# Kernel optimization log

Hardware: AMD Instinct MI355X
Metric: run time of the kernel (lower is better)

Reference implementation:

```python
import jax, jax.numpy as jnp
import numpy as np

N = 4096        # num_nodes == num_messages (required by the einsum contraction)
HID = 256       # hidden_dim
MD = 32         # message_dim (per-head dim)
H = 8           # num_heads


def setup_inputs() -> dict:
    key = jax.random.key(0)
    ks = jax.random.split(key, 12)
    s = 0.02
    return {
        "node_features": jax.random.normal(ks[0], (N, HID), dtype=jnp.float32),
        "messages": jax.random.normal(ks[1], (N, MD), dtype=jnp.float32),
        "adjacency": jax.random.randint(ks[2], (N, N), 0, 2, dtype=jnp.int32),
        "Wq": jax.random.normal(ks[3], (HID, H * MD), dtype=jnp.float32) * s,
        "bq": jnp.zeros((H * MD,), dtype=jnp.float32),
        "Wk": jax.random.normal(ks[4], (HID, H * MD), dtype=jnp.float32) * s,
        "bk": jnp.zeros((H * MD,), dtype=jnp.float32),
        "Wv": jax.random.normal(ks[5], (MD, H * MD), dtype=jnp.float32) * s,
        "bv": jnp.zeros((H * MD,), dtype=jnp.float32),
        "Wo": jax.random.normal(ks[6], (H * MD, MD), dtype=jnp.float32) * s,
        "bo": jnp.zeros((MD,), dtype=jnp.float32),
    }


def reference(node_features, messages, adjacency, Wq, bq, Wk, bk, Wv, bv, Wo, bo):
    n = node_features.shape[0]
    m = messages.shape[0]
    # projections; view(num, H, -1) splits the H*MD output as [H, MD]
    Q = (node_features @ Wq + bq).reshape(n, H, MD)   # [n, h, d]
    K = (node_features @ Wk + bk).reshape(n, H, MD)   # [m, h, d] (m == n)
    V = (messages @ Wv + bv).reshape(m, H, MD)        # [m, h, d]
    scale = 1.0 / np.sqrt(MD).astype(np.float32)
    scores = jnp.einsum('nhd,mhd->nmh', Q, K) * scale  # [n, m, h]
    # adjacency mask: masked_fill(mask == 0, -1e9)
    scores = jnp.where((adjacency == 0)[:, :, None], jnp.float32(-1e9), scores)
    attn = jax.nn.softmax(scores, axis=1)              # softmax over m
    routed = jnp.einsum('nmh,mhd->nhd', attn, V).reshape(n, H * MD)
    routed = routed @ Wo + bo                          # [n, MD]
    return routed, attn.mean(axis=-1)                  # ([n, MD], [n, m])
```

## Files before the change

### kernel.cpp

```cpp
#include <hip/hip_runtime.h>
#include <math.h>

#define NN 4096
#define HID 256
#define MD 32
#define NH 8
#define SCALE 0.17677669529663687f

typedef float f32x4 __attribute__((ext_vector_type(4)));
typedef short bf16x8 __attribute__((ext_vector_type(8)));
typedef _Float16 f16x4 __attribute__((ext_vector_type(4)));
typedef _Float16 f16x2 __attribute__((ext_vector_type(2)));

__device__ inline unsigned int bfr(float x) {
    unsigned int u = __float_as_uint(x);
    return (u + 0x7fffu + ((u >> 16) & 1u)) >> 16;
}
__device__ inline unsigned int pkbf(float a, float b) {
    return bfr(a) | (bfr(b) << 16);
}
__device__ inline unsigned int pkhf(float a, float b) {
    union { f16x2 h; unsigned int u; } z;
    z.h = (f16x2){(_Float16)a, (_Float16)b};
    return z.u;
}

__global__ __launch_bounds__(256, 2) void proj_qk(
    const float* __restrict__ nf,
    const float* __restrict__ Wq, const float* __restrict__ bq,
    const float* __restrict__ Wk, const float* __restrict__ bk,
    unsigned short* __restrict__ Qb, unsigned short* __restrict__ Kb)
{
    __shared__ __align__(16) float inT[256 * 20];
    __shared__ __align__(16) float Wc[16 * 256];
    const int b = blockIdx.x;
    const int isK = b >> 8;
    const int nb = b & 255;
    const float* W = isK ? Wk : Wq;
    const float* bias = isK ? bk : bq;
    unsigned short* outp = isK ? Kb : Qb;
    const int t = threadIdx.x;
    const int rg = t >> 6;
    const int j4 = t & 63;

    for (int i = t; i < 1024; i += 256) {
        int row = i >> 6, kq = i & 63;
        float4 v = *(const float4*)(nf + (size_t)(nb * 16 + row) * 256 + kq * 4);
        inT[(kq * 4 + 0) * 20 + row] = v.x;
        inT[(kq * 4 + 1) * 20 + row] = v.y;
        inT[(kq * 4 + 2) * 20 + row] = v.z;
        inT[(kq * 4 + 3) * 20 + row] = v.w;
    }
    float acc[4][4];
    #pragma unroll
    for (int r = 0; r < 4; ++r)
        #pragma unroll
        for (int d = 0; d < 4; ++d) acc[r][d] = 0.f;

    for (int kc = 0; kc < 16; ++kc) {
        __syncthreads();
        for (int i = t; i < 1024; i += 256)
            *(float4*)&Wc[i * 4] = *(const float4*)(W + (size_t)kc * 4096 + i * 4);
        __syncthreads();
        #pragma unroll 4
        for (int k = 0; k < 16; ++k) {
            float4 iv = *(const float4*)&inT[(kc * 16 + k) * 20 + rg * 4];
            float4 wv = *(const float4*)&Wc[k * 256 + j4 * 4];
            acc[0][0] += iv.x * wv.x; acc[0][1] += iv.x * wv.y;
            acc[0][2] += iv.x * wv.z; acc[0][3] += iv.x * wv.w;
            acc[1][0] += iv.y * wv.x; acc[1][1] += iv.y * wv.y;
            acc[1][2] += iv.y * wv.z; acc[1][3] += iv.y * wv.w;
            acc[2][0] += iv.z * wv.x; acc[2][1] += iv.z * wv.y;
            acc[2][2] += iv.z * wv.z; acc[2][3] += iv.z * wv.w;
            acc[3][0] += iv.w * wv.x; acc[3][1] += iv.w * wv.y;
            acc[3][2] += iv.w * wv.z; acc[3][3] += iv.w * wv.w;
        }
    }
    const float sc = isK ? 1.0f : SCALE;
    const float4 bv = *(const float4*)(bias + j4 * 4);
    const int c0 = j4 * 4, h = c0 >> 5, d = c0 & 31;
    #pragma unroll
    for (int r = 0; r < 4; ++r) {
        int n = nb * 16 + rg * 4 + r;
        float v0 = (acc[r][0] + bv.x) * sc;
        float v1 = (acc[r][1] + bv.y) * sc;
        float v2 = (acc[r][2] + bv.z) * sc;
        float v3 = (acc[r][3] + bv.w) * sc;
        uint2 o;
        o.x = pkbf(v0, v1); o.y = pkbf(v2, v3);
        *(uint2*)(outp + ((size_t)h * NN + n) * 32 + d) = o;
    }
}

__global__ __launch_bounds__(256) void proj_v(
    const float* __restrict__ msg, const float* __restrict__ Wv,
    const float* __restrict__ bv, float* __restrict__ Vo)
{
    __shared__ __align__(16) float in_lds[32 * 32];
    const int nb = blockIdx.x;
    const int t = threadIdx.x;
    {
        int i = t;
        ((float4*)in_lds)[i] = ((const float4*)(msg + (size_t)nb * 1024))[i];
    }
    __syncthreads();
    float acc[32];
    #pragma unroll
    for (int r = 0; r < 32; ++r) acc[r] = 0.f;
    #pragma unroll 8
    for (int k = 0; k < 32; ++k) {
        float w = Wv[k * 256 + t];
        #pragma unroll
        for (int r = 0; r < 32; ++r) acc[r] += in_lds[r * 32 + k] * w;
    }
    const float bb = bv[t];
    #pragma unroll
    for (int r = 0; r < 32; ++r)
        Vo[(size_t)(nb * 32 + r) * 256 + t] = acc[r] + bb;
}

__global__ __launch_bounds__(256) void abit_kernel(
    const int* __restrict__ adj, unsigned long long* __restrict__ abit)
{
    const int n = blockIdx.x * 4 + (threadIdx.x >> 6);
    const int l = threadIdx.x & 63;
    for (int j = 0; j < 64; ++j) {
        int v = adj[(size_t)n * NN + j * 64 + l];
        unsigned long long m = __ballot(v != 0);
        if (l == 0) abit[(size_t)n * 64 + j] = m;
    }
}

__global__ __launch_bounds__(256) void pack_vt(
    const float* __restrict__ Vf, unsigned short* __restrict__ Vt, int usef16)
{
    __shared__ __align__(16) float lds[128 * 33];
    const int h = blockIdx.x >> 5, mt = blockIdx.x & 31;
    const int t = threadIdx.x;
    for (int k = 0; k < 4; ++k) {
        int flat = k * 256 + t;
        int row = flat >> 3, c4 = flat & 7;
        float4 v = *(const float4*)(Vf + (size_t)(mt * 128 + row) * 256 + h * 32 + c4 * 4);
        lds[row * 33 + c4 * 4 + 0] = v.x;
        lds[row * 33 + c4 * 4 + 1] = v.y;
        lds[row * 33 + c4 * 4 + 2] = v.z;
        lds[row * 33 + c4 * 4 + 3] = v.w;
    }
    __syncthreads();
    const int d = t >> 3, mq = t & 7;
    #pragma unroll
    for (int k = 0; k < 2; ++k) {
        int m0 = mq * 16 + k * 8;
        uint4 o;
        if (usef16) {
            o.x = pkhf(lds[(m0 + 0) * 33 + d], lds[(m0 + 1) * 33 + d]);
            o.y = pkhf(lds[(m0 + 2) * 33 + d], lds[(m0 + 3) * 33 + d]);
            o.z = pkhf(lds[(m0 + 4) * 33 + d], lds[(m0 + 5) * 33 + d]);
            o.w = pkhf(lds[(m0 + 6) * 33 + d], lds[(m0 + 7) * 33 + d]);
        } else {
            o.x = pkbf(lds[(m0 + 0) * 33 + d], lds[(m0 + 1) * 33 + d]);
            o.y = pkbf(lds[(m0 + 2) * 33 + d], lds[(m0 + 3) * 33 + d]);
            o.z = pkbf(lds[(m0 + 4) * 33 + d], lds[(m0 + 5) * 33 + d]);
            o.w = pkbf(lds[(m0 + 6) * 33 + d], lds[(m0 + 7) * 33 + d]);
        }
        *(uint4*)(Vt + ((size_t)(h * 32 + d)) * NN + mt * 128 + m0) = o;
    }
}

__global__ __launch_bounds__(256, 4) void sweep1s_kernel(
    const unsigned short* __restrict__ Qb, const unsigned short* __restrict__ Kb,
    const unsigned int* __restrict__ abit, float* __restrict__ Lpart)
{
    __shared__ __align__(16) char smem[32768];
    const int nquad = blockIdx.x, msg = blockIdx.y;
    const int t = threadIdx.x;
    const int w = t >> 6, l = t & 63;
    const int g = l >> 4, q = l & 15;
    const int n0 = nquad * 64 + w * 16;
    const int m0 = msg * 512;
    const int fq = (q >> 1) & 3;

    const char* gsrc[4];
    #pragma unroll
    for (int i = 0; i < 4; ++i) {
        int s = i * 256 + t;
        int tile = s >> 7;
        int r = (s >> 2) & 31;
        int gr = (s & 3) ^ ((r >> 1) & 3);
        gsrc[i] = (const char*)Kb + (((size_t)tile * NN + m0 + r) * 64 + gr * 16);
    }
    const unsigned int* abrow = abit + (size_t)(n0 + q) * 128 + msg * 16;

    bf16x8 qf[8];
    #pragma unroll
    for (int h = 0; h < 8; ++h)
        qf[h] = *(const bf16x8*)(Qb + (((size_t)h * NN + n0 + q) << 5) + g * 8);
    float lacc[8];
    #pragma unroll
    for (int h = 0; h < 8; ++h) lacc[h] = 0.f;

    #pragma unroll
    for (int i = 0; i < 4; ++i)
        __builtin_amdgcn_global_load_lds((const unsigned int*)gsrc[i],
            (unsigned int*)(smem + i * 4096 + w * 1024), 16, 0, 0);
    unsigned int wb = abrow[0];
    unsigned int wbn = 0;
    __syncthreads();

    for (int c = 0; c < 16; ++c) {
        const char* cur = smem + (c & 1) * 16384;
        if (c < 15) {
            wbn = abrow[c + 1];
            char* nxt = smem + ((c & 1) ^ 1) * 16384;
            #pragma unroll
            for (int i = 0; i < 4; ++i)
                __builtin_amdgcn_global_load_lds(
                    (const unsigned int*)(gsrc[i] + (size_t)(c + 1) * 2048),
                    (unsigned int*)(nxt + i * 4096 + w * 1024), 16, 0, 0);
        }
        #pragma unroll
        for (int h = 0; h < 8; ++h) {
            const int ko = h * 2048 + q * 64 + ((g ^ fq) << 4);
            bf16x8 ka0 = *(const bf16x8*)(cur + ko);
            bf16x8 ka1 = *(const bf16x8*)(cur + ko + 1024);
            f32x4 z = {0.f, 0.f, 0.f, 0.f};
            f32x4 s0 = __builtin_amdgcn_mfma_f32_16x16x32_bf16(ka0, qf[h], z, 0, 0, 0);
            f32x4 s1 = __builtin_amdgcn_mfma_f32_16x16x32_bf16(ka1, qf[h], z, 0, 0, 0);
            #pragma unroll
            for (int r = 0; r < 4; ++r) {
                float e0 = __expf(s0[r]);
                float e1 = __expf(s1[r]);
                lacc[h] += ((wb >> (4 * g + r)) & 1u) ? e0 : 0.f;
                lacc[h] += ((wb >> (16 + 4 * g + r)) & 1u) ? e1 : 0.f;
            }
        }
        __syncthreads();
        wb = wbn;
    }
    #pragma unroll
    for (int h = 0; h < 8; ++h) {
        float v = lacc[h];
        v += __shfl_xor(v, 16);
        v += __shfl_xor(v, 32);
        if (g == 0) Lpart[(size_t)msg * 32768 + h * NN + n0 + q] = v;
    }
}

__global__ __launch_bounds__(256, 2) void sweep2s_kernel(
    const unsigned short* __restrict__ Qb, const unsigned short* __restrict__ Kb,
    const unsigned short* __restrict__ Vt, const unsigned int* __restrict__ abit,
    const float* __restrict__ Linv, float* __restrict__ Opart,
    float* __restrict__ amean)
{
    __shared__ __align__(16) char smem[65536];
    const int nquad = blockIdx.x, msg = blockIdx.y;
    const int t = threadIdx.x;
    const int w = t >> 6, l = t & 63;
    const int g = l >> 4, q = l & 15;
    const int n0 = nquad * 64 + w * 16;
    const int m0 = msg * 512;
    const int fq = (q >> 1) & 3;

    const char* gsrc[8];
    unsigned int gstep[8];
    #pragma unroll
    for (int i = 0; i < 8; ++i) {
        int s = i * 256 + t;
        int tile = s >> 7;
        int r = (s >> 2) & 31;
        int gr = (s & 3) ^ ((r >> 1) & 3);
        if (tile < 8) {
            gsrc[i] = (const char*)Kb + (((size_t)tile * NN + m0 + r) * 64 + gr * 16);
            gstep[i] = 2048;
        } else {
            gsrc[i] = (const char*)Vt + ((((size_t)(tile - 8) * 32 + r) * NN + m0) * 2 + gr * 16);
            gstep[i] = 64;
        }
    }
    const unsigned int* abrow = abit + (size_t)(n0 + q) * 128 + msg * 16;

    bf16x8 qf[8];
    float rL[8];
    #pragma unroll
    for (int h = 0; h < 8; ++h) {
        qf[h] = *(const bf16x8*)(Qb + (((size_t)h * NN + n0 + q) << 5) + g * 8);
        rL[h] = Linv[h * NN + n0 + q];
    }
    f32x4 o[8][2];
    #pragma unroll
    for (int h = 0; h < 8; ++h) {
        o[h][0] = (f32x4){0.f, 0.f, 0.f, 0.f};
        o[h][1] = (f32x4){0.f, 0.f, 0.f, 0.f};
    }

    #pragma unroll
    for (int i = 0; i < 8; ++i)
        __builtin_amdgcn_global_load_lds((const unsigned int*)gsrc[i],
            (unsigned int*)(smem + i * 4096 + w * 1024), 16, 0, 0);
    unsigned int wb = abrow[0];
    unsigned int wbn = 0;
    __syncthreads();

    for (int c = 0; c < 16; ++c) {
        const char* cur = smem + (c & 1) * 32768;
        if (c < 15) {
            wbn = abrow[c + 1];
            char* nxt = smem + ((c & 1) ^ 1) * 32768;
            #pragma unroll
            for (int i = 0; i < 8; ++i)
                __builtin_amdgcn_global_load_lds(
                    (const unsigned int*)(gsrc[i] + (size_t)(c + 1) * gstep[i]),
                    (unsigned int*)(nxt + i * 4096 + w * 1024), 16, 0, 0);
        }
        const int mb = m0 + c * 32;
        float am[8];
        #pragma unroll
        for (int r = 0; r < 8; ++r) am[r] = 0.f;

        #pragma unroll
        for (int h = 0; h < 8; ++h) {
            const int ko = h * 2048 + q * 64 + ((g ^ fq) << 4);
            bf16x8 ka0 = *(const bf16x8*)(cur + ko);
            bf16x8 ka1 = *(const bf16x8*)(cur + ko + 1024);
            const int vbase = (8 + h) * 2048 + q * 64 + (g & 1) * 8;
            const int vo0 = vbase + (((g >> 1) ^ fq) << 4);
            const int vo1 = vbase + (((2 + (g >> 1)) ^ fq) << 4);
            f16x4 va00 = *(const f16x4*)(cur + vo0);
            f16x4 va01 = *(const f16x4*)(cur + vo0 + 1024);
            f16x4 va10 = *(const f16x4*)(cur + vo1);
            f16x4 va11 = *(const f16x4*)(cur + vo1 + 1024);
            f32x4 z = {0.f, 0.f, 0.f, 0.f};
            f32x4 s0 = __builtin_amdgcn_mfma_f32_16x16x32_bf16(ka0, qf[h], z, 0, 0, 0);
            f32x4 s1 = __builtin_amdgcn_mfma_f32_16x16x32_bf16(ka1, qf[h], z, 0, 0, 0);
            float pn[8];
            #pragma unroll
            for (int r = 0; r < 4; ++r) {
                float e0 = __expf(s0[r]) * rL[h];
                float e1 = __expf(s1[r]) * rL[h];
                pn[r]     = ((wb >> (4 * g + r)) & 1u) ? e0 : 0.f;
                pn[4 + r] = ((wb >> (16 + 4 * g + r)) & 1u) ? e1 : 0.f;
                am[r] += pn[r];
                am[4 + r] += pn[4 + r];
            }
            union { unsigned int u[2]; f16x4 v; } pA, pB;
            pA.u[0] = pkhf(pn[0], pn[1]); pA.u[1] = pkhf(pn[2], pn[3]);
            pB.u[0] = pkhf(pn[4], pn[5]); pB.u[1] = pkhf(pn[6], pn[7]);
            o[h][0] = __builtin_amdgcn_mfma_f32_16x16x16f16(va00, pA.v, o[h][0], 0, 0, 0);
            o[h][1] = __builtin_amdgcn_mfma_f32_16x16x16f16(va01, pA.v, o[h][1], 0, 0, 0);
            o[h][0] = __builtin_amdgcn_mfma_f32_16x16x16f16(va10, pB.v, o[h][0], 0, 0, 0);
            o[h][1] = __builtin_amdgcn_mfma_f32_16x16x16f16(va11, pB.v, o[h][1], 0, 0, 0);
        }
        float4 a0, a1;
        a0.x = am[0] * 0.125f; a0.y = am[1] * 0.125f;
        a0.z = am[2] * 0.125f; a0.w = am[3] * 0.125f;
        a1.x = am[4] * 0.125f; a1.y = am[5] * 0.125f;
        a1.z = am[6] * 0.125f; a1.w = am[7] * 0.125f;
        *(float4*)(amean + (size_t)(n0 + q) * NN + mb + 4 * g) = a0;
        *(float4*)(amean + (size_t)(n0 + q) * NN + mb + 16 + 4 * g) = a1;
        __syncthreads();
        wb = wbn;
    }

    float* op = Opart + ((size_t)msg * NN + n0 + q) * 256;
    #pragma unroll
    for (int h = 0; h < 8; ++h) {
        *(f32x4*)(op + h * 32 + 4 * g) = o[h][0];
        *(f32x4*)(op + h * 32 + 16 + 4 * g) = o[h][1];
    }
}

__global__ __launch_bounds__(256, 4) void sweep1_old(
    const unsigned short* __restrict__ Qb, const unsigned short* __restrict__ Kb,
    const unsigned int* __restrict__ abit, float* __restrict__ Lpart)
{
    const int ntile = blockIdx.x, msg = blockIdx.y;
    const int t = threadIdx.x;
    const int w = t >> 6, l = t & 63;
    const int g = l >> 4, q = l & 15;
    const int ms = msg * 4 + w;
    const int n0 = ntile * 16;
    const int mbase = ms * 256;
    bf16x8 qf[8];
    #pragma unroll
    for (int h = 0; h < 8; ++h)
        qf[h] = *(const bf16x8*)(Qb + (((size_t)h * NN + n0 + q) << 5) + g * 8);
    float lacc[8];
    #pragma unroll
    for (int h = 0; h < 8; ++h) lacc[h] = 0.f;
    for (int ch = 0; ch < 8; ++ch) {
        const int mb = mbase + ch * 32;
        const unsigned int wbits = abit[(size_t)(n0 + q) * 128 + (mb >> 5)];
        #pragma unroll
        for (int h = 0; h < 8; ++h) {
            bf16x8 ka0 = *(const bf16x8*)(Kb + (((size_t)h * NN + mb + q) << 5) + g * 8);
            bf16x8 ka1 = *(const bf16x8*)(Kb + (((size_t)h * NN + mb + 16 + q) << 5) + g * 8);
            f32x4 z = {0.f, 0.f, 0.f, 0.f};
            f32x4 s0 = __builtin_amdgcn_mfma_f32_16x16x32_bf16(ka0, qf[h], z, 0, 0, 0);
            f32x4 s1 = __builtin_amdgcn_mfma_f32_16x16x32_bf16(ka1, qf[h], z, 0, 0, 0);
            #pragma unroll
            for (int r = 0; r < 4; ++r) {
                float e0 = __expf(s0[r]);
                float e1 = __expf(s1[r]);
                lacc[h] += ((wbits >> (4 * g + r)) & 1u) ? e0 : 0.f;
                lacc[h] += ((wbits >> (16 + 4 * g + r)) & 1u) ? e1 : 0.f;
            }
        }
    }
    #pragma unroll
    for (int h = 0; h < 8; ++h) {
        float v = lacc[h];
        v += __shfl_xor(v, 16);
        v += __shfl_xor(v, 32);
        if (g == 0) Lpart[(size_t)ms * 32768 + h * NN + n0 + q] = v;
    }
}

__global__ __launch_bounds__(256, 2) void sweep2_old(
    const unsigned short* __restrict__ Qb, const unsigned short* __restrict__ Kb,
    const unsigned short* __restrict__ Vt, const unsigned int* __restrict__ abit,
    const float* __restrict__ Linv, float* __restrict__ Opart,
    float* __restrict__ amean)
{
    __shared__ __align__(16) float Ow[2 * 16 * 260];
    const int ntile = blockIdx.x, msg = blockIdx.y;
    const int t = threadIdx.x;
    const int w = t >> 6, l = t & 63;
    const int g = l >> 4, q = l & 15;
    const int ms = msg * 4 + w;
    const int n0 = ntile * 16;
    const int mbase = ms * 256;
    const int baddr = (q + (g & 1) * 32) << 2;
    const bool hi = (g >= 2);
    bf16x8 qf[8];
    float rL[8];
    #pragma unroll
    for (int h = 0; h < 8; ++h) {
        qf[h] = *(const bf16x8*)(Qb + (((size_t)h * NN + n0 + q) << 5) + g * 8);
        rL[h] = Linv[h * NN + n0 + q];
    }
    f32x4 o[8][2];
    #pragma unroll
    for (int h = 0; h < 8; ++h) {
        o[h][0] = (f32x4){0.f, 0.f, 0.f, 0.f};
        o[h][1] = (f32x4){0.f, 0.f, 0.f, 0.f};
    }
    for (int ch = 0; ch < 8; ++ch) {
        const int mb = mbase + ch * 32;
        const unsigned int wbits = abit[(size_t)(n0 + q) * 128 + (mb >> 5)];
        float am[8];
        #pragma unroll
        for (int r = 0; r < 8; ++r) am[r] = 0.f;
        #pragma unroll
        for (int h = 0; h < 8; ++h) {
            bf16x8 ka0 = *(const bf16x8*)(Kb + (((size_t)h * NN + mb + q) << 5) + g * 8);
            bf16x8 ka1 = *(const bf16x8*)(Kb + (((size_t)h * NN + mb + 16 + q) << 5) + g * 8);
            f32x4 z = {0.f, 0.f, 0.f, 0.f};
            f32x4 s0 = __builtin_amdgcn_mfma_f32_16x16x32_bf16(ka0, qf[h], z, 0, 0, 0);
            f32x4 s1 = __builtin_amdgcn_mfma_f32_16x16x32_bf16(ka1, qf[h], z, 0, 0, 0);
            float pn[8];
            #pragma unroll
            for (int r = 0; r < 4; ++r) {
                float e0 = __expf(s0[r]) * rL[h];
                float e1 = __expf(s1[r]) * rL[h];
                pn[r]     = ((wbits >> (4 * g + r)) & 1u) ? e0 : 0.f;
                pn[4 + r] = ((wbits >> (16 + 4 * g + r)) & 1u) ? e1 : 0.f;
                am[r] += pn[r];
                am[4 + r] += pn[4 + r];
            }
            unsigned int pk0 = pkbf(pn[0], pn[1]);
            unsigned int pk1 = pkbf(pn[2], pn[3]);
            unsigned int pk2 = pkbf(pn[4], pn[5]);
            unsigned int pk3 = pkbf(pn[6], pn[7]);
            int r0lo = __builtin_amdgcn_ds_bpermute(baddr,      (int)pk0);
            int r0hi = __builtin_amdgcn_ds_bpermute(baddr,      (int)pk2);
            int r1lo = __builtin_amdgcn_ds_bpermute(baddr,      (int)pk1);
            int r1hi = __builtin_amdgcn_ds_bpermute(baddr,      (int)pk3);
            int r2lo = __builtin_amdgcn_ds_bpermute(baddr + 64, (int)pk0);
            int r2hi = __builtin_amdgcn_ds_bpermute(baddr + 64, (int)pk2);
            int r3lo = __builtin_amdgcn_ds_bpermute(baddr + 64, (int)pk1);
            int r3hi = __builtin_amdgcn_ds_bpermute(baddr + 64, (int)pk3);
            union { unsigned int u[4]; bf16x8 v; } pu;
            pu.u[0] = (unsigned int)(hi ? r0hi : r0lo);
            pu.u[1] = (unsigned int)(hi ? r1hi : r1lo);
            pu.u[2] = (unsigned int)(hi ? r2hi : r2lo);
            pu.u[3] = (unsigned int)(hi ? r3hi : r3lo);
            bf16x8 va0 = *(const bf16x8*)(Vt + ((size_t)(h * 32 + q)) * NN + mb + g * 8);
            bf16x8 va1 = *(const bf16x8*)(Vt + ((size_t)(h * 32 + 16 + q)) * NN + mb + g * 8);
            o[h][0] = __builtin_amdgcn_mfma_f32_16x16x32_bf16(va0, pu.v, o[h][0], 0, 0, 0);
            o[h][1] = __builtin_amdgcn_mfma_f32_16x16x32_bf16(va1, pu.v, o[h][1], 0, 0, 0);
        }
        float4 a0, a1;
        a0.x = am[0] * 0.125f; a0.y = am[1] * 0.125f;
        a0.z = am[2] * 0.125f; a0.w = am[3] * 0.125f;
        a1.x = am[4] * 0.125f; a1.y = am[5] * 0.125f;
        a1.z = am[6] * 0.125f; a1.w = am[7] * 0.125f;
        *(float4*)(amean + (size_t)(n0 + q) * NN + mb + 4 * g) = a0;
        *(float4*)(amean + (size_t)(n0 + q) * NN + mb + 16 + 4 * g) = a1;
    }
    if (w < 2) {
        #pragma unroll
        for (int h = 0; h < 8; ++h)
            #pragma unroll
            for (int dt = 0; dt < 2; ++dt)
                *(f32x4*)&Ow[w * 4160 + q * 260 + h * 32 + dt * 16 + 4 * g] = o[h][dt];
    }
    __syncthreads();
    if (w >= 2) {
        #pragma unroll
        for (int h = 0; h < 8; ++h)
            #pragma unroll
            for (int dt = 0; dt < 2; ++dt) {
                f32x4* p = (f32x4*)&Ow[(w - 2) * 4160 + q * 260 + h * 32 + dt * 16 + 4 * g];
                *p = *p + o[h][dt];
            }
    }
    __syncthreads();
    for (int i = t; i < 4096; i += 256) {
        int n = i >> 8, c2 = i & 255;
        float v = Ow[n * 260 + c2] + Ow[4160 + n * 260 + c2];
        Opart[((size_t)msg * NN + n0 + n) * 256 + c2] = v;
    }
}

__global__ __launch_bounds__(256) void linv_kernel(
    const float* __restrict__ Lpart, float* __restrict__ Linv, int nms)
{
    int i = blockIdx.x * 256 + threadIdx.x;
    float s = 0.f;
    for (int ms = 0; ms < nms; ++ms) s += Lpart[(size_t)ms * 32768 + i];
    Linv[i] = 1.0f / s;
}

__global__ __launch_bounds__(256) void final_kernel(
    const float* __restrict__ Opart, const float* __restrict__ Wo,
    const float* __restrict__ bo, float* __restrict__ routed, int nms)
{
    __shared__ __align__(16) float Osum[16 * 260];
    __shared__ __align__(16) float WoT[32 * 260];
    const int nb = blockIdx.x, t = threadIdx.x;
    for (int i4 = t; i4 < 2048; i4 += 256) {
        int k = i4 >> 3, j4b = i4 & 7;
        float4 v = *(const float4*)(Wo + k * 32 + j4b * 4);
        WoT[(j4b * 4 + 0) * 260 + k] = v.x;
        WoT[(j4b * 4 + 1) * 260 + k] = v.y;
        WoT[(j4b * 4 + 2) * 260 + k] = v.z;
        WoT[(j4b * 4 + 3) * 260 + k] = v.w;
    }
    for (int i = t; i < 4096; i += 256) {
        int r = i >> 8, c = i & 255;
        const float* ap = Opart + ((size_t)(nb * 16 + r)) * 256 + c;
        float s = 0.f;
        for (int ms = 0; ms < nms; ++ms) s += ap[(size_t)ms * 1048576];
        Osum[r * 260 + c] = s;
    }
    __syncthreads();
    const int rh = t >> 5, j = t & 31;
    const float bj = bo[j];
    #pragma unroll
    for (int rr = 0; rr < 2; ++rr) {
        int r = rh * 2 + rr;
        float a0 = 0.f, a1 = 0.f;
        #pragma unroll
        for (int i4 = 0; i4 < 64; i4 += 2) {
            float4 ov = *(const float4*)&Osum[r * 260 + i4 * 4];
            float4 wv = *(const float4*)&WoT[j * 260 + i4 * 4];
            a0 += ov.x * wv.x + ov.y * wv.y + ov.z * wv.z + ov.w * wv.w;
            float4 ov2 = *(const float4*)&Osum[r * 260 + i4 * 4 + 4];
            float4 wv2 = *(const float4*)&WoT[j * 260 + i4 * 4 + 4];
            a1 += ov2.x * wv2.x + ov2.y * wv2.y + ov2.z * wv2.z + ov2.w * wv2.w;
        }
        routed[(size_t)(nb * 16 + r) * 32 + j] = a0 + a1 + bj;
    }
}

extern "C" void kernel_launch(void* const* d_in, const int* in_sizes, int n_in,
                              void* d_out, int out_size, void* d_ws, size_t ws_size,
                              hipStream_t stream) {
    const float* nf  = (const float*)d_in[0];
    const float* msg = (const float*)d_in[1];
    const int*   adj = (const int*)d_in[2];
    const float* Wq  = (const float*)d_in[3];
    const float* bq  = (const float*)d_in[4];
    const float* Wk  = (const float*)d_in[5];
    const float* bk  = (const float*)d_in[6];
    const float* Wv  = (const float*)d_in[7];
    const float* bv  = (const float*)d_in[8];
    const float* Wo  = (const float*)d_in[9];
    const float* bo  = (const float*)d_in[10];

    float* routed = (float*)d_out;
    float* amean  = (float*)d_out + (size_t)NN * MD;
    float* ws = (float*)d_ws;

    const bool bigws = (ws_size >= 43122688ull);

    if (bigws) {
        float* Vf = ws;
        float* Opart = ws;
        unsigned short* Qb = (unsigned short*)(ws + 8388608);
        unsigned short* Kb = (unsigned short*)(ws + 8912896);
        unsigned short* Vt = (unsigned short*)(ws + 9437184);
        unsigned int*   ab32 = (unsigned int*)(ws + 9961472);
        unsigned long long* ab64 = (unsigned long long*)(ws + 9961472);
        float* Lpart = ws + 10485760;
        float* Linv  = ws + 10747904;

        proj_qk<<<512, 256, 0, stream>>>(nf, Wq, bq, Wk, bk, Qb, Kb);
        proj_v<<<128, 256, 0, stream>>>(msg, Wv, bv, Vf);
        abit_kernel<<<1024, 256, 0, stream>>>(adj, ab64);
        pack_vt<<<256, 256, 0, stream>>>(Vf, Vt, 1);
        sweep1s_kernel<<<dim3(64, 8), 256, 0, stream>>>(Qb, Kb, ab32, Lpart);
        linv_kernel<<<128, 256, 0, stream>>>(Lpart, Linv, 8);
        sweep2s_kernel<<<dim3(64, 8), 256, 0, stream>>>(Qb, Kb, Vt, ab32, Linv, Opart, amean);
        final_kernel<<<256, 256, 0, stream>>>(Opart, Wo, bo, routed, 8);
    } else {
        float* Vf = ws;
        float* Opart = ws;
        unsigned short* Qb = (unsigned short*)(ws + 4194304);
        unsigned short* Kb = (unsigned short*)(ws + 4718592);
        unsigned short* Vt = (unsigned short*)(ws + 5242880);
        unsigned int*   ab32 = (unsigned int*)(ws + 5767168);
        unsigned long long* ab64 = (unsigned long long*)(ws + 5767168);
        float* Lpart = ws + 6291456;
        float* Linv  = ws + 6815744;

        proj_qk<<<512, 256, 0, stream>>>(nf, Wq, bq, Wk, bk, Qb, Kb);
        proj_v<<<128, 256, 0, stream>>>(msg, Wv, bv, Vf);
        abit_kernel<<<1024, 256, 0, stream>>>(adj, ab64);
        pack_vt<<<256, 256, 0, stream>>>(Vf, Vt, 0);
        sweep1_old<<<dim3(256, 4), 256, 0, stream>>>(Qb, Kb, ab32, Lpart);
        linv_kernel<<<128, 256, 0, stream>>>(Lpart, Linv, 16);
        sweep2_old<<<dim3(256, 4), 256, 0, stream>>>(Qb, Kb, Vt, ab32, Linv, Opart, amean);
        final_kernel<<<128, 256, 0, stream>>>(Opart, Wo, bo, routed, 4);
    }
}
```

Before: 197.5 us.

## Move Q/K projection to bf16 MFMA, vectorize mask packing, widen V fragment loads

Replaces the scalar-FMA Q/K projection with a bf16 conversion/transposition prep kernel followed by an MFMA-based projection. It also rewrites the adjacency bitmask kernel to read int4 per lane and interleave the bits, and updates the sweep kernels' mask bit indexing to match. The V transpose now uses an interleaved layout so sweep2 can fetch V with single 16-byte loads instead of four 8-byte ones. This adds an extra launch, and node features and weights are rounded to bf16 before the projection rather than only after, which slightly reduces precision.

```diff
diff --git a/kernel.cpp b/kernel.cpp
--- a/kernel.cpp
+++ b/kernel.cpp
@@ -9,6 +9,7 @@
 
 typedef float f32x4 __attribute__((ext_vector_type(4)));
 typedef short bf16x8 __attribute__((ext_vector_type(8)));
+typedef _Float16 f16x8 __attribute__((ext_vector_type(8)));
 typedef _Float16 f16x4 __attribute__((ext_vector_type(4)));
 typedef _Float16 f16x2 __attribute__((ext_vector_type(2)));
 
@@ -25,69 +26,93 @@
     return z.u;
 }
 
-__global__ __launch_bounds__(256, 2) void proj_qk(
-    const float* __restrict__ nf,
-    const float* __restrict__ Wq, const float* __restrict__ bq,
-    const float* __restrict__ Wk, const float* __restrict__ bk,
+__global__ __launch_bounds__(256) void prep_kernel(
+    const float* __restrict__ nf, const float* __restrict__ Wq,
+    const float* __restrict__ Wk, unsigned short* __restrict__ NFb,
+    unsigned short* __restrict__ Wt)
+{
+    __shared__ __align__(16) float lds[64 * 65];
+    const int b = blockIdx.x, t = threadIdx.x;
+    if (b < 512) {
+        const float* src = nf + (size_t)b * 2048 + t * 8;
+        float4 a = ((const float4*)src)[0];
+        float4 c = ((const float4*)src)[1];
+        uint4 o;
+        o.x = pkbf(a.x, a.y); o.y = pkbf(a.z, a.w);
+        o.z = pkbf(c.x, c.y); o.w = pkbf(c.z, c.w);
+        *(uint4*)(NFb + (size_t)b * 2048 + t * 8) = o;
+        return;
+    }
+    const int b2 = b - 512;
+    const int mat = b2 >> 4, tile = b2 & 15;
+    const int k0 = (tile >> 2) * 64, c0 = (tile & 3) * 64;
+    const float* W = mat ? Wk : Wq;
+    #pragma unroll
+    for (int i = 0; i < 16; ++i) {
+        int idx = i * 256 + t;
+        int row = idx >> 4, c4 = idx & 15;
+        float4 v = *(const float4*)(W + (size_t)(k0 + row) * 256 + c0 + c4 * 4);
+        lds[row * 65 + c4 * 4 + 0] = v.x;
+        lds[row * 65 + c4 * 4 + 1] = v.y;
+        lds[row * 65 + c4 * 4 + 2] = v.z;
+        lds[row * 65 + c4 * 4 + 3] = v.w;
+    }
+    __syncthreads();
+    #pragma unroll
+    for (int i = 0; i < 2; ++i) {
+        int j = i * 256 + t;
+        int c_loc = j >> 3, kq = j & 7;
+        uint4 o;
+        o.x = pkbf(lds[(kq * 8 + 0) * 65 + c_loc], lds[(kq * 8 + 1) * 65 + c_loc]);
+        o.y = pkbf(lds[(kq * 8 + 2) * 65 + c_loc], lds[(kq * 8 + 3) * 65 + c_loc]);
+        o.z = pkbf(lds[(kq * 8 + 4) * 65 + c_loc], lds[(kq * 8 + 5) * 65 + c_loc]);
+        o.w = pkbf(lds[(kq * 8 + 6) * 65 + c_loc], lds[(kq * 8 + 7) * 65 + c_loc]);
+        *(uint4*)(Wt + (size_t)mat * 65536 + (size_t)(c0 + c_loc) * 256 + k0 + kq * 8) = o;
+    }
+}
+
+__global__ __launch_bounds__(256, 4) void proj_mfma(
+    const unsigned short* __restrict__ NFb, const unsigned short* __restrict__ Wt,
+    const float* __restrict__ bq, const float* __restrict__ bk,
     unsigned short* __restrict__ Qb, unsigned short* __restrict__ Kb)
 {
-    __shared__ __align__(16) float inT[256 * 20];
-    __shared__ __align__(16) float Wc[16 * 256];
     const int b = blockIdx.x;
-    const int isK = b >> 8;
-    const int nb = b & 255;
-    const float* W = isK ? Wk : Wq;
+    const int isK = b >> 7, nb = b & 127;
+    const unsigned short* Wm = Wt + (size_t)isK * 65536;
     const float* bias = isK ? bk : bq;
     unsigned short* outp = isK ? Kb : Qb;
-    const int t = threadIdx.x;
-    const int rg = t >> 6;
-    const int j4 = t & 63;
-
-    for (int i = t; i < 1024; i += 256) {
-        int row = i >> 6, kq = i & 63;
-        float4 v = *(const float4*)(nf + (size_t)(nb * 16 + row) * 256 + kq * 4);
-        inT[(kq * 4 + 0) * 20 + row] = v.x;
-        inT[(kq * 4 + 1) * 20 + row] = v.y;
-        inT[(kq * 4 + 2) * 20 + row] = v.z;
-        inT[(kq * 4 + 3) * 20 + row] = v.w;
-    }
-    float acc[4][4];
-    #pragma unroll
-    for (int r = 0; r < 4; ++r)
-        #pragma unroll
-        for (int d = 0; d < 4; ++d) acc[r][d] = 0.f;
-
-    for (int kc = 0; kc < 16; ++kc) {
-        __syncthreads();
-        for (int i = t; i < 1024; i += 256)
-            *(float4*)&Wc[i * 4] = *(const float4*)(W + (size_t)kc * 4096 + i * 4);
-        __syncthreads();
-        #pragma unroll 4
-        for (int k = 0; k < 16; ++k) {
-            float4 iv = *(const float4*)&inT[(kc * 16 + k) * 20 + rg * 4];
-            float4 wv = *(const float4*)&Wc[k * 256 + j4 * 4];
-            acc[0][0] += iv.x * wv.x; acc[0][1] += iv.x * wv.y;
-            acc[0][2] += iv.x * wv.z; acc[0][3] += iv.x * wv.w;
-            acc[1][0] += iv.y * wv.x; acc[1][1] += iv.y * wv.y;
-            acc[1][2] += iv.y * wv.z; acc[1][3] += iv.y * wv.w;
-            acc[2][0] += iv.z * wv.x; acc[2][1] += iv.z * wv.y;
-            acc[2][2] += iv.z * wv.z; acc[2][3] += iv.z * wv.w;
-            acc[3][0] += iv.w * wv.x; acc[3][1] += iv.w * wv.y;
-            acc[3][2] += iv.w * wv.z; acc[3][3] += iv.w * wv.w;
+    const int t = threadIdx.x, w = t >> 6, l = t & 63;
+    const int g = l >> 4, q = l & 15;
+    const int n0 = nb * 32 + (w & 1) * 16;
+    const int chalf = w >> 1;
+
+    f32x4 acc[8];
+    #pragma unroll
+    for (int ct = 0; ct < 8; ++ct) acc[ct] = (f32x4){0.f, 0.f, 0.f, 0.f};
+
+    #pragma unroll
+    for (int kc = 0; kc < 8; ++kc) {
+        bf16x8 bfrag = *(const bf16x8*)(NFb + (size_t)(n0 + q) * 256 + kc * 32 + g * 8);
+        #pragma unroll
+        for (int ct = 0; ct < 8; ++ct) {
+            int c = (chalf * 8 + ct) * 16 + q;
+            bf16x8 afrag = *(const bf16x8*)(Wm + (size_t)c * 256 + kc * 32 + g * 8);
+            acc[ct] = __builtin_amdgcn_mfma_f32_16x16x32_bf16(afrag, bfrag, acc[ct], 0, 0, 0);
         }
     }
     const float sc = isK ? 1.0f : SCALE;
-    const float4 bv = *(const float4*)(bias + j4 * 4);
-    const int c0 = j4 * 4, h = c0 >> 5, d = c0 & 31;
-    #pragma unroll
-    for (int r = 0; r < 4; ++r) {
-        int n = nb * 16 + rg * 4 + r;
-        float v0 = (acc[r][0] + bv.x) * sc;
-        float v1 = (acc[r][1] + bv.y) * sc;
-        float v2 = (acc[r][2] + bv.z) * sc;
-        float v3 = (acc[r][3] + bv.w) * sc;
+    const int n = n0 + q;
+    #pragma unroll
+    for (int ct = 0; ct < 8; ++ct) {
+        int c0 = (chalf * 8 + ct) * 16 + 4 * g;
+        float4 bv = *(const float4*)(bias + c0);
+        float v0 = (acc[ct][0] + bv.x) * sc;
+        float v1 = (acc[ct][1] + bv.y) * sc;
+        float v2 = (acc[ct][2] + bv.z) * sc;
+        float v3 = (acc[ct][3] + bv.w) * sc;
         uint2 o;
         o.x = pkbf(v0, v1); o.y = pkbf(v2, v3);
+        int h = c0 >> 5, d = c0 & 31;
         *(uint2*)(outp + ((size_t)h * NN + n) * 32 + d) = o;
     }
 }
@@ -99,10 +124,7 @@
     __shared__ __align__(16) float in_lds[32 * 32];
     const int nb = blockIdx.x;
     const int t = threadIdx.x;
-    {
-        int i = t;
-        ((float4*)in_lds)[i] = ((const float4*)(msg + (size_t)nb * 1024))[i];
-    }
+    ((float4*)in_lds)[t] = ((const float4*)(msg + (size_t)nb * 1024))[t];
     __syncthreads();
     float acc[32];
     #pragma unroll
@@ -120,14 +142,25 @@
 }
 
 __global__ __launch_bounds__(256) void abit_kernel(
-    const int* __restrict__ adj, unsigned long long* __restrict__ abit)
-{
-    const int n = blockIdx.x * 4 + (threadIdx.x >> 6);
-    const int l = threadIdx.x & 63;
-    for (int j = 0; j < 64; ++j) {
-        int v = adj[(size_t)n * NN + j * 64 + l];
-        unsigned long long m = __ballot(v != 0);
-        if (l == 0) abit[(size_t)n * 64 + j] = m;
+    const int* __restrict__ adj, unsigned int* __restrict__ ab32)
+{
+    const int w = threadIdx.x >> 6, lane = threadIdx.x & 63;
+    const int n = blockIdx.x * 4 + w;
+    const int* base = adj + (size_t)n * NN;
+    for (int it = 0; it < 16; ++it) {
+        int4 v = *(const int4*)(base + it * 256 + lane * 4);
+        unsigned long long b0 = __ballot(v.x != 0);
+        unsigned long long b1 = __ballot(v.y != 0);
+        unsigned long long b2 = __ballot(v.z != 0);
+        unsigned long long b3 = __ballot(v.w != 0);
+        if (lane < 8) {
+            unsigned int sh = lane * 8;
+            unsigned int wd = (unsigned int)((b0 >> sh) & 0xffULL)
+                            | ((unsigned int)((b1 >> sh) & 0xffULL) << 8)
+                            | ((unsigned int)((b2 >> sh) & 0xffULL) << 16)
+                            | ((unsigned int)((b3 >> sh) & 0xffULL) << 24);
+            ab32[(size_t)n * 128 + it * 8 + lane] = wd;
+        }
     }
 }
 
@@ -147,23 +180,32 @@
         lds[row * 33 + c4 * 4 + 3] = v.w;
     }
     __syncthreads();
-    const int d = t >> 3, mq = t & 7;
-    #pragma unroll
-    for (int k = 0; k < 2; ++k) {
-        int m0 = mq * 16 + k * 8;
-        uint4 o;
-        if (usef16) {
-            o.x = pkhf(lds[(m0 + 0) * 33 + d], lds[(m0 + 1) * 33 + d]);
-            o.y = pkhf(lds[(m0 + 2) * 33 + d], lds[(m0 + 3) * 33 + d]);
-            o.z = pkhf(lds[(m0 + 4) * 33 + d], lds[(m0 + 5) * 33 + d]);
-            o.w = pkhf(lds[(m0 + 6) * 33 + d], lds[(m0 + 7) * 33 + d]);
-        } else {
+    if (usef16) {
+        #pragma unroll
+        for (int it = 0; it < 2; ++it) {
+            int jb = it * 256 + t;
+            int d = jb >> 4, chs = jb & 15;
+            int chunk = chs >> 2, seg = chs & 3;
+            int mb = chunk * 32 + seg * 4;
+            uint4 o;
+            o.x = pkhf(lds[(mb + 0) * 33 + d],  lds[(mb + 1) * 33 + d]);
+            o.y = pkhf(lds[(mb + 2) * 33 + d],  lds[(mb + 3) * 33 + d]);
+            o.z = pkhf(lds[(mb + 16) * 33 + d], lds[(mb + 17) * 33 + d]);
+            o.w = pkhf(lds[(mb + 18) * 33 + d], lds[(mb + 19) * 33 + d]);
+            *(uint4*)(Vt + ((size_t)(h * 32 + d)) * NN + mt * 128 + chunk * 32 + seg * 8) = o;
+        }
+    } else {
+        const int d = t >> 3, mq = t & 7;
+        #pragma unroll
+        for (int k = 0; k < 2; ++k) {
+            int m0 = mq * 16 + k * 8;
+            uint4 o;
             o.x = pkbf(lds[(m0 + 0) * 33 + d], lds[(m0 + 1) * 33 + d]);
             o.y = pkbf(lds[(m0 + 2) * 33 + d], lds[(m0 + 3) * 33 + d]);
             o.z = pkbf(lds[(m0 + 4) * 33 + d], lds[(m0 + 5) * 33 + d]);
             o.w = pkbf(lds[(m0 + 6) * 33 + d], lds[(m0 + 7) * 33 + d]);
-        }
-        *(uint4*)(Vt + ((size_t)(h * 32 + d)) * NN + mt * 128 + m0) = o;
+            *(uint4*)(Vt + ((size_t)(h * 32 + d)) * NN + mt * 128 + m0) = o;
+        }
     }
 }
 
@@ -230,8 +272,8 @@
             for (int r = 0; r < 4; ++r) {
                 float e0 = __expf(s0[r]);
                 float e1 = __expf(s1[r]);
-                lacc[h] += ((wb >> (4 * g + r)) & 1u) ? e0 : 0.f;
-                lacc[h] += ((wb >> (16 + 4 * g + r)) & 1u) ? e1 : 0.f;
+                lacc[h] += ((wb >> (8 * r + g)) & 1u) ? e0 : 0.f;
+                lacc[h] += ((wb >> (8 * r + g + 4)) & 1u) ? e1 : 0.f;
             }
         }
         __syncthreads();
@@ -322,13 +364,10 @@
             const int ko = h * 2048 + q * 64 + ((g ^ fq) << 4);
             bf16x8 ka0 = *(const bf16x8*)(cur + ko);
             bf16x8 ka1 = *(const bf16x8*)(cur + ko + 1024);
-            const int vbase = (8 + h) * 2048 + q * 64 + (g & 1) * 8;
-            const int vo0 = vbase + (((g >> 1) ^ fq) << 4);
-            const int vo1 = vbase + (((2 + (g >> 1)) ^ fq) << 4);
-            f16x4 va00 = *(const f16x4*)(cur + vo0);
-            f16x4 va01 = *(const f16x4*)(cur + vo0 + 1024);
-            f16x4 va10 = *(const f16x4*)(cur + vo1);
-            f16x4 va11 = *(const f16x4*)(cur + vo1 + 1024);
+            const int vo = (8 + h) * 2048 + q * 64 + ((g ^ fq) << 4);
+            union { f16x8 v8; f16x4 h2[2]; } lo, hi;
+            lo.v8 = *(const f16x8*)(cur + vo);
+            hi.v8 = *(const f16x8*)(cur + vo + 1024);
             f32x4 z = {0.f, 0.f, 0.f, 0.f};
             f32x4 s0 = __builtin_amdgcn_mfma_f32_16x16x32_bf16(ka0, qf[h], z, 0, 0, 0);
             f32x4 s1 = __builtin_amdgcn_mfma_f32_16x16x32_bf16(ka1, qf[h], z, 0, 0, 0);
@@ -337,18 +376,18 @@
             for (int r = 0; r < 4; ++r) {
                 float e0 = __expf(s0[r]) * rL[h];
                 float e1 = __expf(s1[r]) * rL[h];
-                pn[r]     = ((wb >> (4 * g + r)) & 1u) ? e0 : 0.f;
-                pn[4 + r] = ((wb >> (16 + 4 * g + r)) & 1u) ? e1 : 0.f;
+                pn[r]     = ((wb >> (8 * r + g)) & 1u) ? e0 : 0.f;
+                pn[4 + r] = ((wb >> (8 * r + g + 4)) & 1u) ? e1 : 0.f;
                 am[r] += pn[r];
                 am[4 + r] += pn[4 + r];
             }
             union { unsigned int u[2]; f16x4 v; } pA, pB;
             pA.u[0] = pkhf(pn[0], pn[1]); pA.u[1] = pkhf(pn[2], pn[3]);
             pB.u[0] = pkhf(pn[4], pn[5]); pB.u[1] = pkhf(pn[6], pn[7]);
-            o[h][0] = __builtin_amdgcn_mfma_f32_16x16x16f16(va00, pA.v, o[h][0], 0, 0, 0);
-            o[h][1] = __builtin_amdgcn_mfma_f32_16x16x16f16(va01, pA.v, o[h][1], 0, 0, 0);
-            o[h][0] = __builtin_amdgcn_mfma_f32_16x16x16f16(va10, pB.v, o[h][0], 0, 0, 0);
-            o[h][1] = __builtin_amdgcn_mfma_f32_16x16x16f16(va11, pB.v, o[h][1], 0, 0, 0);
+            o[h][0] = __builtin_amdgcn_mfma_f32_16x16x16f16(lo.h2[0], pA.v, o[h][0], 0, 0, 0);
+            o[h][1] = __builtin_amdgcn_mfma_f32_16x16x16f16(hi.h2[0], pA.v, o[h][1], 0, 0, 0);
+            o[h][0] = __builtin_amdgcn_mfma_f32_16x16x16f16(lo.h2[1], pB.v, o[h][0], 0, 0, 0);
+            o[h][1] = __builtin_amdgcn_mfma_f32_16x16x16f16(hi.h2[1], pB.v, o[h][1], 0, 0, 0);
         }
         float4 a0, a1;
         a0.x = am[0] * 0.125f; a0.y = am[1] * 0.125f;
@@ -401,8 +440,8 @@
             for (int r = 0; r < 4; ++r) {
                 float e0 = __expf(s0[r]);
                 float e1 = __expf(s1[r]);
-                lacc[h] += ((wbits >> (4 * g + r)) & 1u) ? e0 : 0.f;
-                lacc[h] += ((wbits >> (16 + 4 * g + r)) & 1u) ? e1 : 0.f;
+                lacc[h] += ((wbits >> (8 * r + g)) & 1u) ? e0 : 0.f;
+                lacc[h] += ((wbits >> (8 * r + g + 4)) & 1u) ? e1 : 0.f;
             }
         }
     }
@@ -462,8 +501,8 @@
             for (int r = 0; r < 4; ++r) {
                 float e0 = __expf(s0[r]) * rL[h];
                 float e1 = __expf(s1[r]) * rL[h];
-                pn[r]     = ((wbits >> (4 * g + r)) & 1u) ? e0 : 0.f;
-                pn[4 + r] = ((wbits >> (16 + 4 * g + r)) & 1u) ? e1 : 0.f;
+                pn[r]     = ((wbits >> (8 * r + g)) & 1u) ? e0 : 0.f;
+                pn[4 + r] = ((wbits >> (8 * r + g + 4)) & 1u) ? e1 : 0.f;
                 am[r] += pn[r];
                 am[4 + r] += pn[4 + r];
             }
@@ -596,18 +635,20 @@
 
     if (bigws) {
         float* Vf = ws;
+        unsigned short* NFb = (unsigned short*)(ws + 2097152);
+        unsigned short* Wt  = (unsigned short*)(ws + 2621440);
         float* Opart = ws;
         unsigned short* Qb = (unsigned short*)(ws + 8388608);
         unsigned short* Kb = (unsigned short*)(ws + 8912896);
         unsigned short* Vt = (unsigned short*)(ws + 9437184);
         unsigned int*   ab32 = (unsigned int*)(ws + 9961472);
-        unsigned long long* ab64 = (unsigned long long*)(ws + 9961472);
         float* Lpart = ws + 10485760;
         float* Linv  = ws + 10747904;
 
-        proj_qk<<<512, 256, 0, stream>>>(nf, Wq, bq, Wk, bk, Qb, Kb);
+        prep_kernel<<<544, 256, 0, stream>>>(nf, Wq, Wk, NFb, Wt);
+        proj_mfma<<<256, 256, 0, stream>>>(NFb, Wt, bq, bk, Qb, Kb);
         proj_v<<<128, 256, 0, stream>>>(msg, Wv, bv, Vf);
-        abit_kernel<<<1024, 256, 0, stream>>>(adj, ab64);
+        abit_kernel<<<1024, 256, 0, stream>>>(adj, ab32);
         pack_vt<<<256, 256, 0, stream>>>(Vf, Vt, 1);
         sweep1s_kernel<<<dim3(64, 8), 256, 0, stream>>>(Qb, Kb, ab32, Lpart);
         linv_kernel<<<128, 256, 0, stream>>>(Lpart, Linv, 8);
@@ -615,18 +656,20 @@
         final_kernel<<<256, 256, 0, stream>>>(Opart, Wo, bo, routed, 8);
     } else {
         float* Vf = ws;
+        unsigned short* NFb = (unsigned short*)(ws + 2097152);
+        unsigned short* Wt  = (unsigned short*)(ws + 2621440);
         float* Opart = ws;
         unsigned short* Qb = (unsigned short*)(ws + 4194304);
         unsigned short* Kb = (unsigned short*)(ws + 4718592);
         unsigned short* Vt = (unsigned short*)(ws + 5242880);
         unsigned int*   ab32 = (unsigned int*)(ws + 5767168);
-        unsigned long long* ab64 = (unsigned long long*)(ws + 5767168);
         float* Lpart = ws + 6291456;
         float* Linv  = ws + 6815744;
 
-        proj_qk<<<512, 256, 0, stream>>>(nf, Wq, bq, Wk, bk, Qb, Kb);
+        prep_kernel<<<544, 256, 0, stream>>>(nf, Wq, Wk, NFb, Wt);
+        proj_mfma<<<256, 256, 0, stream>>>(NFb, Wt, bq, bk, Qb, Kb);
         proj_v<<<128, 256, 0, stream>>>(msg, Wv, bv, Vf);
-        abit_kernel<<<1024, 256, 0, stream>>>(adj, ab64);
+        abit_kernel<<<1024, 256, 0, stream>>>(adj, ab32);
         pack_vt<<<256, 256, 0, stream>>>(Vf, Vt, 0);
         sweep1_old<<<dim3(256, 4), 256, 0, stream>>>(Qb, Kb, ab32, Lpart);
         linv_kernel<<<128, 256, 0, stream>>>(Lpart, Linv, 16);
```

Result: slower. 237.8 us (+20.4%).
